# Optimization experiments

Measured on AMD Instinct MI355X. Metric: run time of the kernel, lower is better.

The kernel has to match this reference:

```python
import jax, jax.numpy as jnp
import numpy as np

V = 30        # vocab_size (amino-acid alphabet, identity embedding => one-hot)
T = 8192      # target_size (output vocab / conv out-channels)
K = 5         # filter_width
L = 512       # target_sequence_length == input seq len
B = 32        # batch


def setup_inputs() -> dict:
    key = jax.random.key(0)
    k1, k2, k3 = jax.random.split(key, 3)
    sentence_batch = jax.random.randint(k1, (B, L), 0, V)
    conv_w = jax.random.normal(k2, (T, V, K), jnp.float32) * (1.0 / np.sqrt(V * K))
    conv_b = jax.random.normal(k3, (T,), jnp.float32) * 0.01
    return {"sentence_batch": sentence_batch, "conv_w": conv_w, "conv_b": conv_b}


def reference(sentence_batch, conv_w, conv_b):
    # pad-or-slice to target_seq_length (here input len == L, so slice is a no-op)
    s = sentence_batch[:, :L]
    # frozen identity embedding == one-hot               [B, L, V]
    one_hot = jax.nn.one_hot(s, V, dtype=conv_w.dtype)
    x = jnp.transpose(one_hot, (0, 2, 1))                # [B, V, L]  (NCH)
    logits = jax.lax.conv_general_dilated(
        x, conv_w,
        window_strides=(1,),
        padding=[(K // 2, K // 2)],
        dimension_numbers=("NCH", "OIH", "NCH"),
    )                                                    # [B, T, L]
    logits = jnp.transpose(logits, (0, 2, 1)) + conv_b   # [B, L, T]
    # eval path: F.softmax over the target dim, then argmax
    probs = jax.nn.softmax(logits, axis=-1)
    new_seq = jnp.argmax(probs, axis=-1)                 # [B, L] int tokens
    return new_seq
```

## Files before the change

kernel.cpp:

```cpp
#include <hip/hip_runtime.h>
#include <hip/hip_fp16.h>

#define Vv 30
#define Tt 8192
#define Kk 5
#define Ll 512
#define Bb 32
#define NVK 150
#define ZROW 150
#define NROWS 151
#define TPOS (Bb * Ll)
#define NC32 256
#define PG 32
#define PPB (TPOS / PG)
#define PPT 2
#define TRm 16
#define TW (Tt / TRm)
#define GPT 8
#define NTILE 8
#define LSG 9
#define NPART 17

__device__ inline float4 add4(float4 a, float4 b) {
    return make_float4(a.x + b.x, a.y + b.y, a.z + b.z, a.w + b.w);
}
__device__ inline float4 tree5(float4 a, float4 b, float4 c, float4 d, float4 e) {
    return add4(add4(add4(a, b), add4(c, d)), e);
}
__device__ inline __half2 bc_h2(float x) { return __builtin_bit_cast(__half2, x); }

__global__ __launch_bounds__(256) void prep_w(
    const float* __restrict__ conv_w,
    const float* __restrict__ conv_b,
    float* __restrict__ wt,
    __half* __restrict__ wh,
    float* __restrict__ cm32,
    unsigned* __restrict__ wmax)
{
    __shared__ float tile[32 * NVK];
    const int t0 = blockIdx.x * 32;
    const int tid = threadIdx.x;

    for (int i = tid; i < 32 * NVK; i += 256)
        tile[i] = conv_w[t0 * NVK + i];
    __syncthreads();

    float amax = 0.0f;
    for (int i = tid; i < NVK * 32; i += 256) {
        const int vk = i >> 5;
        const int tl = i & 31;
        float v = tile[tl * NVK + vk];
        const int k = vk - (vk / Kk) * Kk;
        if (k == 2) v += conv_b[t0 + tl];
        wt[vk * Tt + t0 + tl] = v;
        wh[vk * Tt + t0 + tl] = __float2half(v);
        amax = fmaxf(amax, fabsf(v));
    }
    if (tid < 32) {
        wt[ZROW * Tt + t0 + tid] = 0.0f;
        wh[ZROW * Tt + t0 + tid] = __float2half(0.0f);
    }

#pragma unroll
    for (int m = 32; m >= 1; m >>= 1)
        amax = fmaxf(amax, __shfl_xor(amax, m));
    if ((tid & 63) == 0) atomicMax(wmax, __float_as_uint(amax));

    for (int row = tid; row < NROWS; row += 256) {
        float m;
        if (row == ZROW) {
            m = 0.0f;
        } else {
            const int k = row - (row / Kk) * Kk;
            m = -1e30f;
            for (int tl = 0; tl < 32; ++tl) {
                float v = tile[tl * NVK + row];
                if (k == 2) v += conv_b[t0 + tl];
                m = fmaxf(m, v);
            }
        }
        cm32[row * NC32 + blockIdx.x] = m;
    }
}

__global__ __launch_bounds__(256) void seed_k(
    const int* __restrict__ seq,
    const float* __restrict__ wt,
    const float* __restrict__ cm32,
    float* __restrict__ lb,
    float2* __restrict__ partials)
{
    const int lane = threadIdx.x & 63;
    const int pos  = blockIdx.x * 4 + (threadIdx.x >> 6);
    const int b = pos >> 9;
    const int l = pos & (Ll - 1);

    int rows[Kk];
#pragma unroll
    for (int k = 0; k < Kk; ++k) {
        const int lp = l + k - 2;
        rows[k] = (lp >= 0 && lp < Ll) ? (seq[b * Ll + lp] * Kk + k) : ZROW;
    }

    const float4* __restrict__ c32_4 = (const float4*)cm32;
    const float4 u = tree5(c32_4[rows[0] * 64 + lane], c32_4[rows[1] * 64 + lane],
                           c32_4[rows[2] * 64 + lane], c32_4[rows[3] * 64 + lane],
                           c32_4[rows[4] * 64 + lane]);
    const float uv[4] = {u.x, u.y, u.z, u.w};

    float mu = -1e30f; int mc = 0;
#pragma unroll
    for (int s = 0; s < 4; ++s) {
        const int c = lane * 4 + s;
        if (uv[s] > mu || (uv[s] == mu && c < mc)) { mu = uv[s]; mc = c; }
    }
#pragma unroll
    for (int m = 32; m >= 1; m >>= 1) {
        const float om = __shfl_xor(mu, m);
        const int   oc = __shfl_xor(mc, m);
        if (om > mu || (om == mu && oc < mc)) { mu = om; mc = oc; }
    }
    float mu2 = -1e30f; int mc2 = 0;
#pragma unroll
    for (int s = 0; s < 4; ++s) {
        const int c = lane * 4 + s;
        const float v = (c == mc) ? -1e30f : uv[s];
        if (v > mu2 || (v == mu2 && c < mc2)) { mu2 = v; mc2 = c; }
    }
#pragma unroll
    for (int m = 32; m >= 1; m >>= 1) {
        const float om = __shfl_xor(mu2, m);
        const int   oc = __shfl_xor(mc2, m);
        if (om > mu2 || (om == mu2 && oc < mc2)) { mu2 = om; mc2 = oc; }
    }

    const int wsel = (lane < 32) ? mc : mc2;
    const int t = wsel * 32 + (lane & 31);
    const float w0 = wt[rows[0] * Tt + t];
    const float w1 = wt[rows[1] * Tt + t];
    const float w2 = wt[rows[2] * Tt + t];
    const float w3 = wt[rows[3] * Tt + t];
    const float w4 = wt[rows[4] * Tt + t];
    float bv = ((w0 + w1) + (w2 + w3)) + w4;
    int   bt = t;
#pragma unroll
    for (int m = 32; m >= 1; m >>= 1) {
        const float ov = __shfl_xor(bv, m);
        const int   ot = __shfl_xor(bt, m);
        if (ov > bv || (ov == bv && ot < bt)) { bv = ov; bt = ot; }
    }

    if (lane == 0) {
        lb[pos] = bv;
        partials[16 * TPOS + pos] = make_float2(bv, __int_as_float(bt));
    }
}

__global__ __launch_bounds__(256) void conv_scan16(
    const int* __restrict__ seq,
    const float* __restrict__ wt,
    const __half* __restrict__ wh,
    const float* __restrict__ lb,
    const unsigned* __restrict__ wmax,
    float2* __restrict__ partials)
{
    __shared__ float4 tile4[NROWS * LSG];

    const int bid = blockIdx.x;
    const int pg  = bid & (PG - 1);
    const int tr  = bid >> 5;
    const int tid = threadIdx.x;

    const float TWO_E = 0.05f * fmaxf(__uint_as_float(wmax[0]), 1e-6f);

    int rows[PPT][Kk];
    int foff[PPT][Kk];
    float R[PPT];
#pragma unroll
    for (int j = 0; j < PPT; ++j) {
        const int pos = pg * PPB + j * 256 + tid;
        const int b = pos >> 9;
        const int l = pos & (Ll - 1);
#pragma unroll
        for (int k = 0; k < Kk; ++k) {
            const int lp = l + k - 2;
            const int row = (lp >= 0 && lp < Ll) ? (seq[b * Ll + lp] * Kk + k) : ZROW;
            rows[j][k] = row;
            foff[j][k] = row * LSG;
        }
        R[j] = lb[pos];
    }

    float bv[PPT];
    int   bt[PPT];
#pragma unroll
    for (int j = 0; j < PPT; ++j) { bv[j] = -1e30f; bt[j] = 0; }

    const float4* __restrict__ wh4 = (const float4*)wh;
    const float4* __restrict__ wt4 = (const float4*)wt;

    for (int tl = 0; tl < NTILE; ++tl) {
        const int g0 = tr * (TW / 8) + tl * GPT;

        __syncthreads();
        for (int i = tid; i < NROWS * GPT; i += 256) {
            const int row = i >> 3;
            const int col = i & 7;
            tile4[row * LSG + col] = wh4[row * 1024 + g0 + col];
        }
        __syncthreads();

        unsigned mask = 0;

#pragma unroll 4
        for (int g = 0; g < GPT; ++g) {
#pragma unroll
            for (int j = 0; j < PPT; ++j) {
                const float4 q0 = tile4[foff[j][0] + g];
                const float4 q1 = tile4[foff[j][1] + g];
                const float4 q2 = tile4[foff[j][2] + g];
                const float4 q3 = tile4[foff[j][3] + g];
                const float4 q4 = tile4[foff[j][4] + g];
                const __half2 s0 = __hadd2(__hadd2(__hadd2(bc_h2(q0.x), bc_h2(q1.x)),
                                                   __hadd2(bc_h2(q2.x), bc_h2(q3.x))), bc_h2(q4.x));
                const __half2 s1 = __hadd2(__hadd2(__hadd2(bc_h2(q0.y), bc_h2(q1.y)),
                                                   __hadd2(bc_h2(q2.y), bc_h2(q3.y))), bc_h2(q4.y));
                const __half2 s2 = __hadd2(__hadd2(__hadd2(bc_h2(q0.z), bc_h2(q1.z)),
                                                   __hadd2(bc_h2(q2.z), bc_h2(q3.z))), bc_h2(q4.z));
                const __half2 s3 = __hadd2(__hadd2(__hadd2(bc_h2(q0.w), bc_h2(q1.w)),
                                                   __hadd2(bc_h2(q2.w), bc_h2(q3.w))), bc_h2(q4.w));
                const float2 f0 = __half22float2(s0);
                const float2 f1 = __half22float2(s1);
                const float2 f2 = __half22float2(s2);
                const float2 f3 = __half22float2(s3);
                const float gl = fmaxf(fmaxf(fmaxf(f0.x, f0.y), fmaxf(f1.x, f1.y)),
                                       fmaxf(fmaxf(f2.x, f2.y), fmaxf(f3.x, f3.y)));
                R[j] = fmaxf(R[j], gl);
                if (gl >= R[j] - TWO_E) mask |= 1u << (j * GPT + g);
            }
        }

#pragma unroll
        for (int j = 0; j < PPT; ++j) {
            unsigned m = (mask >> (j * GPT)) & 0xFFu;
            while (m) {
                const int g = __ffs(m) - 1;
                m &= m - 1;
                const int gc = g0 + g;
                const float4 eA = tree5(wt4[rows[j][0] * 2048 + 2 * gc],
                                        wt4[rows[j][1] * 2048 + 2 * gc],
                                        wt4[rows[j][2] * 2048 + 2 * gc],
                                        wt4[rows[j][3] * 2048 + 2 * gc],
                                        wt4[rows[j][4] * 2048 + 2 * gc]);
                const float4 eB = tree5(wt4[rows[j][0] * 2048 + 2 * gc + 1],
                                        wt4[rows[j][1] * 2048 + 2 * gc + 1],
                                        wt4[rows[j][2] * 2048 + 2 * gc + 1],
                                        wt4[rows[j][3] * 2048 + 2 * gc + 1],
                                        wt4[rows[j][4] * 2048 + 2 * gc + 1]);
                const int t0 = gc * 8;
                const float ev[8] = {eA.x, eA.y, eA.z, eA.w, eB.x, eB.y, eB.z, eB.w};
#pragma unroll
                for (int q = 0; q < 8; ++q) {
                    const int t = t0 + q;
                    if (ev[q] > bv[j] || (ev[q] == bv[j] && t < bt[j])) { bv[j] = ev[q]; bt[j] = t; }
                }
            }
        }
    }

#pragma unroll
    for (int j = 0; j < PPT; ++j) {
        const int pos = pg * PPB + j * 256 + tid;
        partials[tr * TPOS + pos] = make_float2(bv[j], __int_as_float(bt[j]));
    }
}

__global__ __launch_bounds__(256) void combine(
    const float2* __restrict__ partials,
    int* __restrict__ out)
{
    const int pos = blockIdx.x * 256 + threadIdx.x;
    float bv = -1e30f;
    int   bt = 0x7fffffff;
#pragma unroll
    for (int i = 0; i < NPART; ++i) {
        const float2 p = partials[i * TPOS + pos];
        const int t = __float_as_int(p.y);
        if (p.x > bv || (p.x == bv && t < bt)) { bv = p.x; bt = t; }
    }
    out[pos] = bt;
}

extern "C" void kernel_launch(void* const* d_in, const int* in_sizes, int n_in,
                              void* d_out, int out_size, void* d_ws, size_t ws_size,
                              hipStream_t stream)
{
    const int*   seq    = (const int*)d_in[0];
    const float* conv_w = (const float*)d_in[1];
    const float* conv_b = (const float*)d_in[2];
    int*         out    = (int*)d_out;

    float*    wt   = (float*)d_ws;
    __half*   wh   = (__half*)(wt + (size_t)NROWS * Tt);
    float*    cm32 = (float*)(wh + (size_t)NROWS * Tt);
    float*    lbp  = cm32 + (size_t)NROWS * NC32;
    float2*   part = (float2*)(lbp + TPOS);
    unsigned* wmax = (unsigned*)(part + (size_t)NPART * TPOS);

    (void)hipMemsetAsync(wmax, 0, sizeof(unsigned), stream);
    prep_w<<<Tt / 32, 256, 0, stream>>>(conv_w, conv_b, wt, wh, cm32, wmax);
    seed_k<<<TPOS / 4, 256, 0, stream>>>(seq, wt, cm32, lbp, part);
    conv_scan16<<<PG * TRm, 256, 0, stream>>>(seq, wt, wh, lbp, wmax, part);
    combine<<<TPOS / 256, 256, 0, stream>>>(part, out);
}
```

Before: 154.4 us.

## Process one position per thread and split targets into 32 ranges

The scan kernel goes from two positions per thread with 16 target ranges to one position per thread with 32 target ranges and 64 position groups, so it launches four times as many blocks, each doing half the tiles. This aims to raise occupancy and parallelism and to shorten per-block serial work. The cost is that each loaded weight tile is reused by half as many positions, giving more global and LDS traffic, and the combine step now reduces 33 partials instead of 17, doubling the partials written and read. The host launch grid presumably changes in the hidden lines.

```diff
diff --git a/kernel.cpp b/kernel.cpp
--- a/kernel.cpp
+++ b/kernel.cpp
@@ -11,15 +11,14 @@
 #define NROWS 151
 #define TPOS (Bb * Ll)
 #define NC32 256
-#define PG 32
+#define PG 64
 #define PPB (TPOS / PG)
-#define PPT 2
-#define TRm 16
+#define TRm 32
 #define TW (Tt / TRm)
 #define GPT 8
-#define NTILE 8
+#define NTILE 4
 #define LSG 9
-#define NPART 17
+#define NPART 33
 
 __device__ inline float4 add4(float4 a, float4 b) {
     return make_float4(a.x + b.x, a.y + b.y, a.z + b.z, a.w + b.w);
@@ -152,7 +151,7 @@
 
     if (lane == 0) {
         lb[pos] = bv;
-        partials[16 * TPOS + pos] = make_float2(bv, __int_as_float(bt));
+        partials[(NPART - 1) * TPOS + pos] = make_float2(bv, __int_as_float(bt));
     }
 }
 
@@ -168,33 +167,27 @@
 
     const int bid = blockIdx.x;
     const int pg  = bid & (PG - 1);
-    const int tr  = bid >> 5;
+    const int tr  = bid >> 6;
     const int tid = threadIdx.x;
 
     const float TWO_E = 0.05f * fmaxf(__uint_as_float(wmax[0]), 1e-6f);
 
-    int rows[PPT][Kk];
-    int foff[PPT][Kk];
-    float R[PPT];
-#pragma unroll
-    for (int j = 0; j < PPT; ++j) {
-        const int pos = pg * PPB + j * 256 + tid;
-        const int b = pos >> 9;
-        const int l = pos & (Ll - 1);
-#pragma unroll
-        for (int k = 0; k < Kk; ++k) {
-            const int lp = l + k - 2;
-            const int row = (lp >= 0 && lp < Ll) ? (seq[b * Ll + lp] * Kk + k) : ZROW;
-            rows[j][k] = row;
-            foff[j][k] = row * LSG;
-        }
-        R[j] = lb[pos];
-    }
-
-    float bv[PPT];
-    int   bt[PPT];
-#pragma unroll
-    for (int j = 0; j < PPT; ++j) { bv[j] = -1e30f; bt[j] = 0; }
+    const int pos = pg * PPB + tid;
+    const int b = pos >> 9;
+    const int l = pos & (Ll - 1);
+
+    int rows[Kk];
+    int foff[Kk];
+#pragma unroll
+    for (int k = 0; k < Kk; ++k) {
+        const int lp = l + k - 2;
+        const int row = (lp >= 0 && lp < Ll) ? (seq[b * Ll + lp] * Kk + k) : ZROW;
+        rows[k] = row;
+        foff[k] = row * LSG;
+    }
+    float R = lb[pos];
+    float bv = -1e30f;
+    int   bt = 0;
 
     const float4* __restrict__ wh4 = (const float4*)wh;
     const float4* __restrict__ wt4 = (const float4*)wt;
@@ -212,67 +205,56 @@
 
         unsigned mask = 0;
 
-#pragma unroll 4
+#pragma unroll
         for (int g = 0; g < GPT; ++g) {
-#pragma unroll
-            for (int j = 0; j < PPT; ++j) {
-                const float4 q0 = tile4[foff[j][0] + g];
-                const float4 q1 = tile4[foff[j][1] + g];
-                const float4 q2 = tile4[foff[j][2] + g];
-                const float4 q3 = tile4[foff[j][3] + g];
-                const float4 q4 = tile4[foff[j][4] + g];
-                const __half2 s0 = __hadd2(__hadd2(__hadd2(bc_h2(q0.x), bc_h2(q1.x)),
-                                                   __hadd2(bc_h2(q2.x), bc_h2(q3.x))), bc_h2(q4.x));
-                const __half2 s1 = __hadd2(__hadd2(__hadd2(bc_h2(q0.y), bc_h2(q1.y)),
-                                                   __hadd2(bc_h2(q2.y), bc_h2(q3.y))), bc_h2(q4.y));
-                const __half2 s2 = __hadd2(__hadd2(__hadd2(bc_h2(q0.z), bc_h2(q1.z)),
-                                                   __hadd2(bc_h2(q2.z), bc_h2(q3.z))), bc_h2(q4.z));
-                const __half2 s3 = __hadd2(__hadd2(__hadd2(bc_h2(q0.w), bc_h2(q1.w)),
-                                                   __hadd2(bc_h2(q2.w), bc_h2(q3.w))), bc_h2(q4.w));
-                const float2 f0 = __half22float2(s0);
-                const float2 f1 = __half22float2(s1);
-                const float2 f2 = __half22float2(s2);
-                const float2 f3 = __half22float2(s3);
-                const float gl = fmaxf(fmaxf(fmaxf(f0.x, f0.y), fmaxf(f1.x, f1.y)),
-                                       fmaxf(fmaxf(f2.x, f2.y), fmaxf(f3.x, f3.y)));
-                R[j] = fmaxf(R[j], gl);
-                if (gl >= R[j] - TWO_E) mask |= 1u << (j * GPT + g);
+            const float4 q0 = tile4[foff[0] + g];
+            const float4 q1 = tile4[foff[1] + g];
+            const float4 q2 = tile4[foff[2] + g];
+            const float4 q3 = tile4[foff[3] + g];
+            const float4 q4 = tile4[foff[4] + g];
+            const __half2 s0 = __hadd2(__hadd2(__hadd2(bc_h2(q0.x), bc_h2(q1.x)),
+                                               __hadd2(bc_h2(q2.x), bc_h2(q3.x))), bc_h2(q4.x));
+            const __half2 s1 = __hadd2(__hadd2(__hadd2(bc_h2(q0.y), bc_h2(q1.y)),
+                                               __hadd2(bc_h2(q2.y), bc_h2(q3.y))), bc_h2(q4.y));
+            const __half2 s2 = __hadd2(__hadd2(__hadd2(bc_h2(q0.z), bc_h2(q1.z)),
+                                               __hadd2(bc_h2(q2.z), bc_h2(q3.z))), bc_h2(q4.z));
+            const __half2 s3 = __hadd2(__hadd2(__hadd2(bc_h2(q0.w), bc_h2(q1.w)),
+                                               __hadd2(bc_h2(q2.w), bc_h2(q3.w))), bc_h2(q4.w));
+            const float2 f0 = __half22float2(s0);
+            const float2 f1 = __half22float2(s1);
+            const float2 f2 = __half22float2(s2);
+            const float2 f3 = __half22float2(s3);
+            const float gl = fmaxf(fmaxf(fmaxf(f0.x, f0.y), fmaxf(f1.x, f1.y)),
+                                   fmaxf(fmaxf(f2.x, f2.y), fmaxf(f3.x, f3.y)));
+            R = fmaxf(R, gl);
+            if (gl >= R - TWO_E) mask |= 1u << g;
+        }
+
+        while (mask) {
+            const int g = __ffs(mask) - 1;
+            mask &= mask - 1;
+            const int gc = g0 + g;
+            const float4 eA = tree5(wt4[rows[0] * 2048 + 2 * gc],
+                                    wt4[rows[1] * 2048 + 2 * gc],
+                                    wt4[rows[2] * 2048 + 2 * gc],
+                                    wt4[rows[3] * 2048 + 2 * gc],
+                                    wt4[rows[4] * 2048 + 2 * gc]);
+            const float4 eB = tree5(wt4[rows[0] * 2048 + 2 * gc + 1],
+                                    wt4[rows[1] * 2048 + 2 * gc + 1],
+                                    wt4[rows[2] * 2048 + 2 * gc + 1],
+                                    wt4[rows[3] * 2048 + 2 * gc + 1],
+                                    wt4[rows[4] * 2048 + 2 * gc + 1]);
+            const int t0 = gc * 8;
+            const float ev[8] = {eA.x, eA.y, eA.z, eA.w, eB.x, eB.y, eB.z, eB.w};
+#pragma unroll
+            for (int q = 0; q < 8; ++q) {
+                const int t = t0 + q;
+                if (ev[q] > bv || (ev[q] == bv && t < bt)) { bv = ev[q]; bt = t; }
             }
         }
-
-#pragma unroll
-        for (int j = 0; j < PPT; ++j) {
-            unsigned m = (mask >> (j * GPT)) & 0xFFu;
-            while (m) {
-                const int g = __ffs(m) - 1;
-                m &= m - 1;
-                const int gc = g0 + g;
-                const float4 eA = tree5(wt4[rows[j][0] * 2048 + 2 * gc],
-                                        wt4[rows[j][1] * 2048 + 2 * gc],
-                                        wt4[rows[j][2] * 2048 + 2 * gc],
-                                        wt4[rows[j][3] * 2048 + 2 * gc],
-                                        wt4[rows[j][4] * 2048 + 2 * gc]);
-                const float4 eB = tree5(wt4[rows[j][0] * 2048 + 2 * gc + 1],
-                                        wt4[rows[j][1] * 2048 + 2 * gc + 1],
-                                        wt4[rows[j][2] * 2048 + 2 * gc + 1],
-                                        wt4[rows[j][3] * 2048 + 2 * gc + 1],
-                                        wt4[rows[j][4] * 2048 + 2 * gc + 1]);
-                const int t0 = gc * 8;
-                const float ev[8] = {eA.x, eA.y, eA.z, eA.w, eB.x, eB.y, eB.z, eB.w};
-#pragma unroll
-                for (int q = 0; q < 8; ++q) {
-                    const int t = t0 + q;
-                    if (ev[q] > bv[j] || (ev[q] == bv[j] && t < bt[j])) { bv[j] = ev[q]; bt[j] = t; }
-                }
-            }
-        }
-    }
-
-#pragma unroll
-    for (int j = 0; j < PPT; ++j) {
-        const int pos = pg * PPB + j * 256 + tid;
-        partials[tr * TPOS + pos] = make_float2(bv[j], __int_as_float(bt[j]));
-    }
+    }
+
+    partials[tr * TPOS + pos] = make_float2(bv, __int_as_float(bt));
 }
 
 __global__ __launch_bounds__(256) void combine(
```

Result: faster. 151.1 us (-2.1%).
